# Performance work log

Measured on AMD Instinct MI355X. Metric: run time of the kernel, lower is better.

## Reference

```python
import jax, jax.numpy as jnp
import numpy as np

H, HKV, DH = 32, 8, 128
ROPE_BASE = 500000.0


def _rope(x, pos):
    # x: [B, H, T, D]; MLX non-traditional rope (split halves)
    D = x.shape[-1]
    half = D // 2
    freqs = ROPE_BASE ** (-(jnp.arange(half, dtype=jnp.float32) * 2.0 / D))  # [half]
    t = pos + jnp.arange(x.shape[2], dtype=jnp.float32)                      # [T]
    ang = t[:, None] * freqs[None, :]                                        # [T, half]
    cos, sin = jnp.cos(ang), jnp.sin(ang)
    x1, x2 = x[..., :half], x[..., half:]
    return jnp.concatenate([x1 * cos - x2 * sin, x1 * sin + x2 * cos], axis=-1)


def setup_inputs() -> dict:
    key = jax.random.key(0)
    ks = jax.random.split(key, 5)
    B, T, HID = 1, 2048, 4096
    s = 0.02
    return {
        "hidden_states": jax.random.normal(ks[0], (B, T, HID), jnp.float32),
        "Wq": jax.random.normal(ks[1], (H * DH, HID), jnp.float32) * s,
        "Wk": jax.random.normal(ks[2], (HKV * DH, HID), jnp.float32) * s,
        "Wv": jax.random.normal(ks[3], (HKV * DH, HID), jnp.float32) * s,
        "Wo": jax.random.normal(ks[4], (HID, H * DH), jnp.float32) * s,
        "k_cache": jnp.zeros((1, HKV, 4096, DH), jnp.float32),
        "v_cache": jnp.zeros((1, HKV, 4096, DH), jnp.float32),
        "pos_int": 0,
    }


def reference(hidden_states, Wq, Wk, Wv, Wo, k_cache, v_cache, pos_int):
    B, T, _ = hidden_states.shape
    # QKV projections (no bias, Llama-style) -> [B, h, T, D]
    q = (hidden_states @ Wq.T).reshape(B, T, H, DH).transpose(0, 2, 1, 3)
    k = (hidden_states @ Wk.T).reshape(B, T, HKV, DH).transpose(0, 2, 1, 3)
    v = (hidden_states @ Wv.T).reshape(B, T, HKV, DH).transpose(0, 2, 1, 3)
    # RoPE with position offset
    q = _rope(q, pos_int)
    k = _rope(k, pos_int)
    # KV-cache scatter update at pos_int, then window to [:pos_int+T]
    k_cache = jax.lax.dynamic_update_slice(k_cache, k, (0, 0, pos_int, 0))
    v_cache = jax.lax.dynamic_update_slice(v_cache, v, (0, 0, pos_int, 0))
    Tk = pos_int + T
    k_win = k_cache[:, :, :Tk, :]
    v_win = v_cache[:, :, :Tk, :]
    # GQA: repeat_interleave KV heads to match query heads
    group = H // HKV
    k_ = jnp.repeat(k_win, group, axis=1)   # [B, H, Tk, D]
    v_ = jnp.repeat(v_win, group, axis=1)
    # SDPA, is_causal=True => top-left aligned causal mask (query i sees keys j<=i)
    scale = 1.0 / jnp.sqrt(jnp.asarray(DH, jnp.float32))
    scores = jnp.einsum("bhtd,bhsd->bhts", q, k_) * scale  # [B, H, T, Tk]
    causal = jnp.arange(Tk)[None, :] <= jnp.arange(T)[:, None]
    scores = jnp.where(causal[None, None], scores, jnp.finfo(scores.dtype).min)
    attn = jax.nn.softmax(scores, axis=-1)
    out = jnp.einsum("bhts,bhsd->bhtd", attn, v_)           # [B, H, T, D]
    out = out.transpose(0, 2, 1, 3).reshape(B, T, H * DH)
    return out @ Wo.T
```

## Files before the change

### kernel.cpp

```cpp
#include <hip/hip_runtime.h>


#define DEVI __device__ __forceinline__

typedef __attribute__((ext_vector_type(8))) short short8;
typedef __attribute__((ext_vector_type(4))) float f32x4;

DEVI unsigned short f2bf(float f) {
  union { float f; unsigned u; } x; x.f = f;
  unsigned r = x.u + 0x7FFFu + ((x.u >> 16) & 1u);
  return (unsigned short)(r >> 16);
}
DEVI float bf2f(unsigned short h) {
  union { unsigned u; float f; } x; x.u = ((unsigned)h) << 16;
  return x.f;
}
DEVI f32x4 mfma16(short8 a, short8 b, f32x4 c) {
  return __builtin_amdgcn_mfma_f32_16x16x32_bf16(a, b, c, 0, 0, 0);
}
DEVI void gl2lds16(const unsigned short* g, unsigned short* l) {
  __builtin_amdgcn_global_load_lds(
      (const __attribute__((address_space(1))) unsigned int*)g,
      (__attribute__((address_space(3))) unsigned int*)l, 16, 0, 0);
}
DEVI void bar() { __builtin_amdgcn_s_barrier(); }
DEVI void sfence() { __builtin_amdgcn_sched_barrier(0); }

DEVI void cvt_region(const float* __restrict__ src,
                     unsigned short* __restrict__ dst, int n4, int start,
                     int stride) {
  for (int i = start; i < n4; i += stride) {
    float4 v = ((const float4*)src)[i];
    ushort4 h;
    h.x = f2bf(v.x); h.y = f2bf(v.y); h.z = f2bf(v.z); h.w = f2bf(v.w);
    ((ushort4*)dst)[i] = h;
  }
}
__global__ __launch_bounds__(256)
void cvt5_kernel(const float* __restrict__ s0, const float* __restrict__ s1,
                 const float* __restrict__ s2, const float* __restrict__ s3,
                 const float* __restrict__ s4,
                 unsigned short* __restrict__ d0, unsigned short* __restrict__ d1,
                 unsigned short* __restrict__ d2, unsigned short* __restrict__ d3,
                 unsigned short* __restrict__ d4,
                 int n0, int n1, int n2, int n3, int n4) {
  const int start = blockIdx.x * 256 + threadIdx.x;
  const int stride = gridDim.x * 256;
  cvt_region(s0, d0, n0, start, stride);
  cvt_region(s1, d1, n1, start, stride);
  cvt_region(s2, d2, n2, start, stride);
  cvt_region(s3, d3, n3, start, stride);
  cvt_region(s4, d4, n4, start, stride);
}

__global__ __launch_bounds__(512, 2)
void gemm_qkv_8ph(const unsigned short* __restrict__ hsb,
                  const unsigned short* __restrict__ Wqb,
                  const unsigned short* __restrict__ Wkb,
                  const unsigned short* __restrict__ Wvb,
                  unsigned short* __restrict__ Qb,
                  unsigned short* __restrict__ Kb,
                  unsigned short* __restrict__ Vb) {
  const int K = 4096;
  const int NT = 64;
  __shared__ __align__(16) unsigned short Ls[2][2][2][256][32];
  const int tid = threadIdx.x, lane = tid & 63, w = tid >> 6;
  const int wr = w >> 2, wc = w & 3;
  const int m0 = blockIdx.y * 256;
  const int n0g = blockIdx.x * 256;

  const unsigned short* Bsrc; unsigned short* outp; int ldo, oc;
  if (n0g < 4096)      { Bsrc = Wqb + (size_t)n0g * K;          outp = Qb; ldo = 4096; oc = n0g; }
  else if (n0g < 5120) { Bsrc = Wkb + (size_t)(n0g - 4096) * K; outp = Kb; ldo = 1024; oc = n0g - 4096; }
  else                 { Bsrc = Wvb + (size_t)(n0g - 5120) * K; outp = Vb; ldo = 1024; oc = n0g - 5120; }
  const unsigned short* Asrc = hsb + (size_t)m0 * K;

  auto stageU = [&](const unsigned short* src, int ab, int kh, int tt, int bb) {
#pragma unroll
    for (int j = 0; j < 2; ++j) {
      const int seg = j * 8 + w;
      const int row = seg * 16 + (lane >> 2);
      const int cs  = (lane & 3) ^ ((row >> 1) & 3);
      gl2lds16(src + (size_t)row * K + tt * 64 + kh * 32 + cs * 8,
               &Ls[bb][ab][kh][seg * 16][0]);
    }
  };
  auto ldA = [&](int bb, int kh, int fm) -> short8 {
    const int ra = wr * 128 + fm * 16 + (lane & 15);
    const int cs = (lane >> 4) ^ ((ra >> 1) & 3);
    return *(const short8*)&Ls[bb][0][kh][ra][cs * 8];
  };
  auto ldB = [&](int bb, int kh, int fn) -> short8 {
    const int rb = wc * 64 + fn * 16 + (lane & 15);
    const int cs = (lane >> 4) ^ ((rb >> 1) & 3);
    return *(const short8*)&Ls[bb][1][kh][rb][cs * 8];
  };

  f32x4 acc[8][4];
#pragma unroll
  for (int i = 0; i < 8; ++i)
#pragma unroll
    for (int j = 0; j < 4; ++j) acc[i][j] = (f32x4){0.f, 0.f, 0.f, 0.f};

  stageU(Asrc, 0, 0, 0, 0);
  stageU(Asrc, 0, 1, 0, 0);
  stageU(Bsrc, 1, 0, 0, 0);
  stageU(Bsrc, 1, 1, 0, 0);
  stageU(Bsrc, 1, 0, 1, 1);
  stageU(Asrc, 0, 0, 1, 1);
  stageU(Bsrc, 1, 1, 1, 1);
  asm volatile("s_waitcnt vmcnt(6)" ::: "memory");
  bar();
  sfence();

  short8 af[4], bfr[4];
  for (int t = 0; t < NT; ++t) {
    const int bb = t & 1, nb = bb ^ 1;
#pragma unroll
    for (int i = 0; i < 4; ++i) af[i] = ldA(bb, 0, i);
#pragma unroll
    for (int i = 0; i < 4; ++i) bfr[i] = ldB(bb, 0, i);
    if (t + 1 < NT) stageU(Asrc, 0, 1, t + 1, nb);
    bar();
    __builtin_amdgcn_s_setprio(1);
#pragma unroll
    for (int i = 0; i < 4; ++i)
#pragma unroll
      for (int j = 0; j < 4; ++j) acc[i][j] = mfma16(af[i], bfr[j], acc[i][j]);
    __builtin_amdgcn_s_setprio(0);
    sfence(); bar(); sfence();
#pragma unroll
    for (int i = 0; i < 4; ++i) af[i] = ldA(bb, 0, 4 + i);
    if (t + 2 < NT) stageU(Bsrc, 1, 0, t + 2, bb);
    bar();
    __builtin_amdgcn_s_setprio(1);
#pragma unroll
    for (int i = 0; i < 4; ++i)
#pragma unroll
      for (int j = 0; j < 4; ++j) acc[4 + i][j] = mfma16(af[i], bfr[j], acc[4 + i][j]);
    __builtin_amdgcn_s_setprio(0);
    sfence(); bar(); sfence();
#pragma unroll
    for (int i = 0; i < 4; ++i) af[i] = ldA(bb, 1, i);
#pragma unroll
    for (int i = 0; i < 4; ++i) bfr[i] = ldB(bb, 1, i);
    if (t + 2 < NT) stageU(Asrc, 0, 0, t + 2, bb);
    bar();
    __builtin_amdgcn_s_setprio(1);
#pragma unroll
    for (int i = 0; i < 4; ++i)
#pragma unroll
      for (int j = 0; j < 4; ++j) acc[i][j] = mfma16(af[i], bfr[j], acc[i][j]);
    __builtin_amdgcn_s_setprio(0);
    sfence(); bar(); sfence();
#pragma unroll
    for (int i = 0; i < 4; ++i) af[i] = ldA(bb, 1, 4 + i);
    if (t + 2 < NT) stageU(Bsrc, 1, 1, t + 2, bb);
    bar();
    __builtin_amdgcn_s_setprio(1);
#pragma unroll
    for (int i = 0; i < 4; ++i)
#pragma unroll
      for (int j = 0; j < 4; ++j) acc[4 + i][j] = mfma16(af[i], bfr[j], acc[4 + i][j]);
    __builtin_amdgcn_s_setprio(0);
    if (t < NT - 2) asm volatile("s_waitcnt vmcnt(6)" ::: "memory");
    else            asm volatile("s_waitcnt vmcnt(0)" ::: "memory");
    sfence(); bar(); sfence();
  }

#pragma unroll
  for (int fm = 0; fm < 8; ++fm) {
    const int rb0 = m0 + wr * 128 + fm * 16 + ((lane >> 4) << 2);
#pragma unroll
    for (int fn = 0; fn < 4; ++fn) {
      const int cb = oc + wc * 64 + fn * 16 + (lane & 15);
#pragma unroll
      for (int r = 0; r < 4; ++r)
        outp[(size_t)(rb0 + r) * ldo + cb] = f2bf(acc[fm][fn][r]);
    }
  }
}

__global__ __launch_bounds__(256)
void postproc_kernel(const unsigned short* __restrict__ Vb,
                     unsigned short* __restrict__ VtG,
                     unsigned short* __restrict__ Qb,
                     unsigned short* __restrict__ Kb,
                     const int* __restrict__ posp) {
  __shared__ unsigned short tile[64][68];
  const int b = blockIdx.x, tid = threadIdx.x;
  if (b < 512) {
    const int t0 = (b & 31) * 64;
    const int c0 = (b >> 5) * 64;
    const int r = tid >> 4;
    const int c4 = (tid & 15) << 2;
#pragma unroll
    for (int i = 0; i < 4; ++i) {
      ushort4 v = *(const ushort4*)(Vb + (size_t)(t0 + r + i * 16) * 1024 + c0 + c4);
      *(ushort4*)&tile[r + i * 16][c4] = v;
    }
    __syncthreads();
#pragma unroll
    for (int i = 0; i < 4; ++i) {
      int d = r + i * 16;
      ushort4 o;
      o.x = tile[c4 + 0][d]; o.y = tile[c4 + 1][d];
      o.z = tile[c4 + 2][d]; o.w = tile[c4 + 3][d];
      *(ushort4*)(VtG + (size_t)(c0 + d) * 2048 + t0 + c4) = o;
    }
    return;
  }
  const int QP = 2048 * 32 * 64;
  const int KP = 2048 * 8 * 64;
  int idx = (b - 512) * 256 + tid;
  if (idx >= QP + KP) return;
  unsigned short* base; int t, hh, d, ld;
  if (idx < QP) {
    base = Qb; ld = 4096;
    t = idx >> 11; int rem = idx & 2047; hh = rem >> 6; d = rem & 63;
  } else {
    int j = idx - QP; base = Kb; ld = 1024;
    t = j >> 9; int rem = j & 511; hh = rem >> 6; d = rem & 63;
  }
  float freq = exp2f(-(float)d * 0.29580575880077f);
  float ang = (float)(t + posp[0]) * freq;
  float s, c;
  __sincosf(ang, &s, &c);
  size_t i1 = (size_t)t * ld + hh * 128 + d;
  float x1 = bf2f(base[i1]), x2 = bf2f(base[i1 + 64]);
  base[i1]      = f2bf(x1 * c - x2 * s);
  base[i1 + 64] = f2bf(x1 * s + x2 * c);
}

__global__ __launch_bounds__(512)
void attn_kernel(const unsigned short* __restrict__ Qb,
                 const unsigned short* __restrict__ Kb,
                 const unsigned short* __restrict__ VtG,
                 unsigned short* __restrict__ Ob) {
  __shared__ __align__(16) unsigned short Ks[128][128];
  __shared__ __align__(16) unsigned short Vt[128][128];
  __shared__ __align__(16) unsigned short Ps[8][16][128];
  const int tid = threadIdx.x, lane = tid & 63, w = tid >> 6;
  const int h = blockIdx.y;
  const int qt = (blockIdx.y >> 4) ? (15 - blockIdx.x) : blockIdx.x;
  const int kh = h >> 2;
  const int q0 = qt * 128;
  const float SCALE = 0.08838834764831845f;

  short8 aq[4];
  {
    const int qrow = q0 + w * 16 + (lane & 15);
#pragma unroll
    for (int ks = 0; ks < 4; ++ks)
      aq[ks] = *(const short8*)(Qb + (size_t)qrow * 4096 + h * 128 + ks * 32 +
                                ((lane >> 4) << 3));
  }

  f32x4 o_acc[8];
#pragma unroll
  for (int n8 = 0; n8 < 8; ++n8) o_acc[n8] = (f32x4){0.f, 0.f, 0.f, 0.f};
  float mst[4], lst[4];
#pragma unroll
  for (int r = 0; r < 4; ++r) { mst[r] = -1e30f; lst[r] = 0.f; }

  const int ntiles = qt + 1;
  for (int st = 0; st < ntiles; ++st) {
    const int s0 = st * 128;
#pragma unroll
    for (int j = 0; j < 4; ++j) {
      int sr = w * 16 + j * 4 + (lane >> 4);
      int sc = (((lane & 15) << 4) ^ ((sr & 7) << 4)) >> 1;
      gl2lds16(Kb + (size_t)(s0 + sr) * 1024 + kh * 128 + sc, &Ks[w * 16 + j * 4][0]);
    }
#pragma unroll
    for (int j = 0; j < 4; ++j) {
      int dr = w * 16 + j * 4 + (lane >> 4);
      int sc = (((lane & 15) << 4) ^ ((dr & 7) << 4)) >> 1;
      gl2lds16(VtG + (size_t)(kh * 128 + dr) * 2048 + s0 + sc, &Vt[w * 16 + j * 4][0]);
    }
    __syncthreads();

    f32x4 sacc[8];
#pragma unroll
    for (int ni = 0; ni < 8; ++ni) sacc[ni] = (f32x4){0.f, 0.f, 0.f, 0.f};
#pragma unroll
    for (int ks = 0; ks < 4; ++ks) {
      const int co = ks * 64 + ((lane >> 4) << 4);
      short8 bk[8];
#pragma unroll
      for (int ni = 0; ni < 8; ++ni) {
        int kr = ni * 16 + (lane & 15);
        bk[ni] = *(const short8*)((const char*)(&Ks[kr][0]) + (co ^ ((kr & 7) << 4)));
      }
#pragma unroll
      for (int ni = 0; ni < 8; ++ni)
        sacc[ni] = mfma16(aq[ks], bk[ni], sacc[ni]);
    }

    char* pb = (char*)(&Ps[w][0][0]);
#pragma unroll
    for (int r = 0; r < 4; ++r) {
      const int qrow = q0 + w * 16 + ((lane >> 4) << 2) + r;
      float v8[8]; float vmax = -1e30f;
#pragma unroll
      for (int ni = 0; ni < 8; ++ni) {
        int scol = s0 + ni * 16 + (lane & 15);
        float x = sacc[ni][r] * SCALE;
        if (scol > qrow) x = -1e30f;
        v8[ni] = x; vmax = fmaxf(vmax, x);
      }
      vmax = fmaxf(vmax, __shfl_xor(vmax, 1));
      vmax = fmaxf(vmax, __shfl_xor(vmax, 2));
      vmax = fmaxf(vmax, __shfl_xor(vmax, 4));
      vmax = fmaxf(vmax, __shfl_xor(vmax, 8));
      float mo = mst[r];
      float mn = fmaxf(mo, vmax);
      float al = __expf(mo - mn);
      float rs = 0.f;
      const int prow = ((lane >> 4) << 2) + r;
      const int pswz = ((prow >> 2) & 3) << 5;
#pragma unroll
      for (int ni = 0; ni < 8; ++ni) {
        float p = __expf(v8[ni] - mn);
        rs += p;
        int cbyte = (ni * 16 + (lane & 15)) * 2;
        *(unsigned short*)(pb + prow * 256 + (cbyte ^ pswz)) = f2bf(p);
      }
      rs += __shfl_xor(rs, 1);
      rs += __shfl_xor(rs, 2);
      rs += __shfl_xor(rs, 4);
      rs += __shfl_xor(rs, 8);
      lst[r] = lst[r] * al + rs;
      mst[r] = mn;
#pragma unroll
      for (int n8 = 0; n8 < 8; ++n8) o_acc[n8][r] *= al;
    }

#pragma unroll
    for (int ks2 = 0; ks2 < 4; ++ks2) {
      const int co = ks2 * 64 + ((lane >> 4) << 4);
      const int pr = lane & 15;
      short8 pa = *(const short8*)(pb + pr * 256 + (co ^ (((pr >> 2) & 3) << 5)));
#pragma unroll
      for (int n8 = 0; n8 < 8; ++n8) {
        int vr = n8 * 16 + (lane & 15);
        short8 bv = *(const short8*)((const char*)(&Vt[vr][0]) + (co ^ ((vr & 7) << 4)));
        o_acc[n8] = mfma16(pa, bv, o_acc[n8]);
      }
    }
    __syncthreads();
  }

#pragma unroll
  for (int r = 0; r < 4; ++r) {
    float inv = 1.0f / lst[r];
    int row = q0 + w * 16 + ((lane >> 4) << 2) + r;
#pragma unroll
    for (int n8 = 0; n8 < 8; ++n8)
      Ob[(size_t)row * 4096 + h * 128 + n8 * 16 + (lane & 15)] =
          f2bf(o_acc[n8][r] * inv);
  }
}

__global__ __launch_bounds__(256, 2)
void gemm_out_bf16(const unsigned short* __restrict__ Ab,
                   const unsigned short* __restrict__ Wob,
                   float* __restrict__ Cout) {
  const int K = 4096;
  __shared__ __align__(16) unsigned short As[128][64];
  __shared__ __align__(16) unsigned short Bs[128][64];
  const int tid = threadIdx.x, lane = tid & 63, wid = tid >> 6;
  const int m0 = blockIdx.y * 128;
  const int n0 = blockIdx.x * 128;
  const unsigned short* Asrc = Ab + (size_t)m0 * K;
  const unsigned short* Bsrc = Wob + (size_t)n0 * K;

  f32x4 acc[4][4];
#pragma unroll
  for (int i = 0; i < 4; ++i)
#pragma unroll
    for (int j = 0; j < 4; ++j) acc[i][j] = (f32x4){0.f, 0.f, 0.f, 0.f};

  const int wm = (wid >> 1) * 64, wn = (wid & 1) * 64;
  const int srow = wid * 32 + (lane >> 3);
  const int scol = (lane & 7) * 8;

  for (int k0 = 0; k0 < K; k0 += 64) {
#pragma unroll
    for (int i = 0; i < 4; ++i) {
      gl2lds16(Asrc + (size_t)(srow + i * 8) * K + k0 + scol, &As[wid * 32 + i * 8][0]);
      gl2lds16(Bsrc + (size_t)(srow + i * 8) * K + k0 + scol, &Bs[wid * 32 + i * 8][0]);
    }
    __syncthreads();
#pragma unroll
    for (int ks = 0; ks < 2; ++ks) {
      short8 af[4], bfr[4];
      const int co = ks * 64 + ((lane >> 4) << 4);
#pragma unroll
      for (int i = 0; i < 4; ++i) {
        af[i]  = *(const short8*)((const char*)(&As[wm + i * 16 + (lane & 15)][0]) + co);
        bfr[i] = *(const short8*)((const char*)(&Bs[wn + i * 16 + (lane & 15)][0]) + co);
      }
#pragma unroll
      for (int i = 0; i < 4; ++i)
#pragma unroll
        for (int j = 0; j < 4; ++j)
          acc[i][j] = mfma16(af[i], bfr[j], acc[i][j]);
    }
    __syncthreads();
  }

#pragma unroll
  for (int i = 0; i < 4; ++i) {
    int rb = m0 + wm + i * 16 + ((lane >> 4) << 2);
#pragma unroll
    for (int j = 0; j < 4; ++j) {
      int cb = n0 + wn + j * 16 + (lane & 15);
#pragma unroll
      for (int r = 0; r < 4; ++r)
        Cout[(size_t)(rb + r) * 4096 + cb] = acc[i][j][r];
    }
  }
}

extern "C" void kernel_launch(void* const* d_in, const int* in_sizes, int n_in,
                              void* d_out, int out_size, void* d_ws, size_t ws_size,
                              hipStream_t stream) {
  const float* hs = (const float*)d_in[0];
  const float* Wq = (const float*)d_in[1];
  const float* Wk = (const float*)d_in[2];
  const float* Wv = (const float*)d_in[3];
  const float* Wo = (const float*)d_in[4];
  const int* pos = (const int*)d_in[7];

  unsigned short* hsb = (unsigned short*)d_ws;
  unsigned short* Wqb = hsb + (size_t)8  * 1024 * 1024;
  unsigned short* Wkb = Wqb + (size_t)16 * 1024 * 1024;
  unsigned short* Wvb = Wkb + (size_t)4  * 1024 * 1024;
  unsigned short* Wob = Wvb + (size_t)4  * 1024 * 1024;
  unsigned short* Qb  = Wob + (size_t)16 * 1024 * 1024;
  unsigned short* Kb  = Qb  + (size_t)8  * 1024 * 1024;
  unsigned short* Vb  = Kb  + (size_t)2  * 1024 * 1024;
  unsigned short* Ob  = Vb  + (size_t)2  * 1024 * 1024;
  unsigned short* VtG = hsb;
  float* out = (float*)d_out;

  cvt5_kernel<<<dim3(2048), 256, 0, stream>>>(
      hs, Wq, Wk, Wv, Wo, hsb, Wqb, Wkb, Wvb, Wob,
      2 * 1024 * 1024, 4 * 1024 * 1024, 1 * 1024 * 1024, 1 * 1024 * 1024,
      4 * 1024 * 1024);

  gemm_qkv_8ph<<<dim3(24, 8), 512, 0, stream>>>(hsb, Wqb, Wkb, Wvb, Qb, Kb, Vb);

  const int npairs = 2048 * 32 * 64 + 2048 * 8 * 64;
  const int rope_blocks = (npairs + 255) / 256;
  postproc_kernel<<<dim3(512 + rope_blocks), 256, 0, stream>>>(Vb, VtG, Qb, Kb, pos);

  attn_kernel<<<dim3(16, 32), 512, 0, stream>>>(Qb, Kb, VtG, Ob);
  gemm_out_bf16<<<dim3(32, 16), 256, 0, stream>>>(Ob, Wob, out);
}
```

Baseline: 366.9 us.

## Double-buffer attention KV tiles and remap block indices for XCD locality

The attention kernel now uses 64-key tiles with double-buffered K/V in LDS. It prefetches the next tile with async global-to-LDS loads, synchronises through explicit vmcnt waits and barriers, and no longer fully stalls on each tile load. All three compute kernels switch to 1D grids whose block-index decode places blocks that share weights or KV heads on the same XCD (bid&7), aiming for better L2 reuse. Attention also reorders query tiles to balance causal work across blocks. Smaller tiles double the loop iterations and softmax rescale overhead.

```diff
diff --git a/kernel.cpp b/kernel.cpp
--- a/kernel.cpp
+++ b/kernel.cpp
@@ -66,8 +66,9 @@
   __shared__ __align__(16) unsigned short Ls[2][2][2][256][32];
   const int tid = threadIdx.x, lane = tid & 63, w = tid >> 6;
   const int wr = w >> 2, wc = w & 3;
-  const int m0 = blockIdx.y * 256;
-  const int n0g = blockIdx.x * 256;
+  const int bid = blockIdx.x;
+  const int m0 = (bid & 7) * 256;
+  const int n0g = (bid >> 3) * 256;
 
   const unsigned short* Bsrc; unsigned short* outp; int ldo, oc;
   if (n0g < 4096)      { Bsrc = Wqb + (size_t)n0g * K;          outp = Qb; ldo = 4096; oc = n0g; }
@@ -237,13 +238,15 @@
                  const unsigned short* __restrict__ Kb,
                  const unsigned short* __restrict__ VtG,
                  unsigned short* __restrict__ Ob) {
-  __shared__ __align__(16) unsigned short Ks[128][128];
-  __shared__ __align__(16) unsigned short Vt[128][128];
-  __shared__ __align__(16) unsigned short Ps[8][16][128];
+  __shared__ __align__(16) unsigned short Ks[2][64][128];
+  __shared__ __align__(16) unsigned short Vt[2][128][64];
+  __shared__ __align__(16) unsigned short Ps[8][16][64];
   const int tid = threadIdx.x, lane = tid & 63, w = tid >> 6;
-  const int h = blockIdx.y;
-  const int qt = (blockIdx.y >> 4) ? (15 - blockIdx.x) : blockIdx.x;
-  const int kh = h >> 2;
+  const int b = blockIdx.x;
+  const int kh = b & 7;
+  const int h  = kh * 4 + ((b >> 3) & 3);
+  const int qi = b >> 5;
+  const int qt = (qi < 8) ? qi : 23 - qi;
   const int q0 = qt * 128;
   const float SCALE = 0.08838834764831845f;
 
@@ -263,37 +266,51 @@
 #pragma unroll
   for (int r = 0; r < 4; ++r) { mst[r] = -1e30f; lst[r] = 0.f; }
 
-  const int ntiles = qt + 1;
+  auto stage = [&](int st, int bb) {
+    const int s0 = st * 64;
+#pragma unroll
+    for (int j = 0; j < 2; ++j) {
+      int sr = w * 8 + j * 4 + (lane >> 4);
+      int sc = (((lane & 15) << 4) ^ ((sr & 7) << 4)) >> 1;
+      gl2lds16(Kb + (size_t)(s0 + sr) * 1024 + kh * 128 + sc,
+               &Ks[bb][w * 8 + j * 4][0]);
+    }
+#pragma unroll
+    for (int j = 0; j < 2; ++j) {
+      int dr = w * 16 + j * 8 + (lane >> 3);
+      int sc = (((lane & 7) << 4) ^ ((dr & 7) << 4)) >> 1;
+      gl2lds16(VtG + (size_t)(kh * 128 + dr) * 2048 + s0 + sc,
+               &Vt[bb][w * 16 + j * 8][0]);
+    }
+  };
+
+  const int ntiles = 2 * (qt + 1);
+  stage(0, 0);
   for (int st = 0; st < ntiles; ++st) {
-    const int s0 = st * 128;
-#pragma unroll
-    for (int j = 0; j < 4; ++j) {
-      int sr = w * 16 + j * 4 + (lane >> 4);
-      int sc = (((lane & 15) << 4) ^ ((sr & 7) << 4)) >> 1;
-      gl2lds16(Kb + (size_t)(s0 + sr) * 1024 + kh * 128 + sc, &Ks[w * 16 + j * 4][0]);
-    }
-#pragma unroll
-    for (int j = 0; j < 4; ++j) {
-      int dr = w * 16 + j * 4 + (lane >> 4);
-      int sc = (((lane & 15) << 4) ^ ((dr & 7) << 4)) >> 1;
-      gl2lds16(VtG + (size_t)(kh * 128 + dr) * 2048 + s0 + sc, &Vt[w * 16 + j * 4][0]);
-    }
-    __syncthreads();
-
-    f32x4 sacc[8];
-#pragma unroll
-    for (int ni = 0; ni < 8; ++ni) sacc[ni] = (f32x4){0.f, 0.f, 0.f, 0.f};
+    const int cb = st & 1;
+    const int s0 = st * 64;
+    if (st + 1 < ntiles) {
+      stage(st + 1, cb ^ 1);
+      asm volatile("s_waitcnt vmcnt(4)" ::: "memory");
+    } else {
+      asm volatile("s_waitcnt vmcnt(0)" ::: "memory");
+    }
+    bar(); sfence();
+
+    f32x4 sacc[4];
+#pragma unroll
+    for (int ni = 0; ni < 4; ++ni) sacc[ni] = (f32x4){0.f, 0.f, 0.f, 0.f};
 #pragma unroll
     for (int ks = 0; ks < 4; ++ks) {
       const int co = ks * 64 + ((lane >> 4) << 4);
-      short8 bk[8];
-#pragma unroll
-      for (int ni = 0; ni < 8; ++ni) {
+      short8 bk[4];
+#pragma unroll
+      for (int ni = 0; ni < 4; ++ni) {
         int kr = ni * 16 + (lane & 15);
-        bk[ni] = *(const short8*)((const char*)(&Ks[kr][0]) + (co ^ ((kr & 7) << 4)));
+        bk[ni] = *(const short8*)((const char*)(&Ks[cb][kr][0]) + (co ^ ((kr & 7) << 4)));
       }
 #pragma unroll
-      for (int ni = 0; ni < 8; ++ni)
+      for (int ni = 0; ni < 4; ++ni)
         sacc[ni] = mfma16(aq[ks], bk[ni], sacc[ni]);
     }
 
@@ -301,13 +318,13 @@
 #pragma unroll
     for (int r = 0; r < 4; ++r) {
       const int qrow = q0 + w * 16 + ((lane >> 4) << 2) + r;
-      float v8[8]; float vmax = -1e30f;
-#pragma unroll
-      for (int ni = 0; ni < 8; ++ni) {
+      float v4[4]; float vmax = -1e30f;
+#pragma unroll
+      for (int ni = 0; ni < 4; ++ni) {
         int scol = s0 + ni * 16 + (lane & 15);
         float x = sacc[ni][r] * SCALE;
         if (scol > qrow) x = -1e30f;
-        v8[ni] = x; vmax = fmaxf(vmax, x);
+        v4[ni] = x; vmax = fmaxf(vmax, x);
       }
       vmax = fmaxf(vmax, __shfl_xor(vmax, 1));
       vmax = fmaxf(vmax, __shfl_xor(vmax, 2));
@@ -320,11 +337,11 @@
       const int prow = ((lane >> 4) << 2) + r;
       const int pswz = ((prow >> 2) & 3) << 5;
 #pragma unroll
-      for (int ni = 0; ni < 8; ++ni) {
-        float p = __expf(v8[ni] - mn);
+      for (int ni = 0; ni < 4; ++ni) {
+        float p = __expf(v4[ni] - mn);
         rs += p;
         int cbyte = (ni * 16 + (lane & 15)) * 2;
-        *(unsigned short*)(pb + prow * 256 + (cbyte ^ pswz)) = f2bf(p);
+        *(unsigned short*)(pb + prow * 128 + (cbyte ^ pswz)) = f2bf(p);
       }
       rs += __shfl_xor(rs, 1);
       rs += __shfl_xor(rs, 2);
@@ -337,18 +354,18 @@
     }
 
 #pragma unroll
-    for (int ks2 = 0; ks2 < 4; ++ks2) {
+    for (int ks2 = 0; ks2 < 2; ++ks2) {
       const int co = ks2 * 64 + ((lane >> 4) << 4);
       const int pr = lane & 15;
-      short8 pa = *(const short8*)(pb + pr * 256 + (co ^ (((pr >> 2) & 3) << 5)));
+      short8 pa = *(const short8*)(pb + pr * 128 + (co ^ (((pr >> 2) & 3) << 5)));
 #pragma unroll
       for (int n8 = 0; n8 < 8; ++n8) {
         int vr = n8 * 16 + (lane & 15);
-        short8 bv = *(const short8*)((const char*)(&Vt[vr][0]) + (co ^ ((vr & 7) << 4)));
+        short8 bv = *(const short8*)((const char*)(&Vt[cb][vr][0]) + (co ^ ((vr & 7) << 4)));
         o_acc[n8] = mfma16(pa, bv, o_acc[n8]);
       }
     }
-    __syncthreads();
+    sfence(); bar(); sfence();
   }
 
 #pragma unroll
@@ -370,8 +387,9 @@
   __shared__ __align__(16) unsigned short As[128][64];
   __shared__ __align__(16) unsigned short Bs[128][64];
   const int tid = threadIdx.x, lane = tid & 63, wid = tid >> 6;
-  const int m0 = blockIdx.y * 128;
-  const int n0 = blockIdx.x * 128;
+  const int bid = blockIdx.x;
+  const int m0 = (((bid & 7) + 8 * (bid >> 8))) * 128;
+  const int n0 = ((bid >> 3) & 31) * 128;
   const unsigned short* Asrc = Ab + (size_t)m0 * K;
   const unsigned short* Bsrc = Wob + (size_t)n0 * K;
 
@@ -450,12 +468,12 @@
       2 * 1024 * 1024, 4 * 1024 * 1024, 1 * 1024 * 1024, 1 * 1024 * 1024,
       4 * 1024 * 1024);
 
-  gemm_qkv_8ph<<<dim3(24, 8), 512, 0, stream>>>(hsb, Wqb, Wkb, Wvb, Qb, Kb, Vb);
+  gemm_qkv_8ph<<<dim3(192), 512, 0, stream>>>(hsb, Wqb, Wkb, Wvb, Qb, Kb, Vb);
 
   const int npairs = 2048 * 32 * 64 + 2048 * 8 * 64;
   const int rope_blocks = (npairs + 255) / 256;
   postproc_kernel<<<dim3(512 + rope_blocks), 256, 0, stream>>>(Vb, VtG, Qb, Kb, pos);
 
-  attn_kernel<<<dim3(16, 32), 512, 0, stream>>>(Qb, Kb, VtG, Ob);
-  gemm_out_bf16<<<dim3(32, 16), 256, 0, stream>>>(Ob, Wob, out);
-}
+  attn_kernel<<<dim3(512), 512, 0, stream>>>(Qb, Kb, VtG, Ob);
+  gemm_out_bf16<<<dim3(512), 256, 0, stream>>>(Ob, Wob, out);
+}
```

New measurement: 359.7 us. No clear change (-2.0%).
